# Optimization experiments

Measured on AMD Instinct MI355X. Metric: run time of the kernel, lower is better.

## Reference

```python
import jax, jax.numpy as jnp
import numpy as np

A = 4096      # alleles
RPA = 20      # mean reads per allele
R = A * RPA   # total reads per data source
C = 12        # input channels (pileup features)
L = 32        # read window length
D = 32        # hidden feature dim
NOUT = 2


def setup_inputs() -> dict:
    key = jax.random.key(0)
    k = jax.random.split(key, 8)
    # ragged read counts per allele (alternating 16/24, mean 20, sums to R)
    counts0 = np.tile(np.array([16, 24], dtype=np.int64), A // 2)
    counts1 = np.tile(np.array([24, 16], dtype=np.int64), A // 2)
    return {
        "tensors0": jax.random.normal(k[0], (R, C, L), dtype=jnp.float32),
        "tensors1": jax.random.normal(k[1], (R, C, L), dtype=jnp.float32),
        "W0": jax.random.normal(k[2], (D, C), dtype=jnp.float32) * 0.1,
        "b0": jnp.zeros((D,), dtype=jnp.float32),
        "W1": jax.random.normal(k[3], (D, C), dtype=jnp.float32) * 0.1,
        "b1": jnp.zeros((D,), dtype=jnp.float32),
        "W2": jax.random.normal(k[4], (NOUT, 2 * D), dtype=jnp.float32) * 0.1,
        "b2": jnp.zeros((NOUT,), dtype=jnp.float32),
        "numReadsPerAllele0": jnp.asarray(counts0),
        "numReadsPerAllele1": jnp.asarray(counts1),
        "numAllelesPerSite": jnp.full((A // 2,), 2, dtype=jnp.int64),
        "depthMultiplier0": jnp.asarray(counts0, dtype=jnp.float32),
        "depthMultiplier1": jnp.asarray(counts1, dtype=jnp.float32),
    }


def _frames(t, W, b):
    # pointwise read-feature extractor: [R,C,L] -> [R,D,L]
    return jax.nn.relu(jnp.einsum('rcl,dc->rdl', t, W) + b[None, :, None])


def reference(tensors0, tensors1, W0, b0, W1, b1, W2, b2,
              numReadsPerAllele0, numReadsPerAllele1,
              numAllelesPerSite, depthMultiplier0, depthMultiplier1):
    nA = numReadsPerAllele0.shape[0]
    nR = tensors0.shape[0]
    # segment ids replace torch.split + per-segment torch.sum (ragged segment-sum)
    seg0 = jnp.repeat(jnp.arange(nA), numReadsPerAllele0, total_repeat_length=nR)
    seg1 = jnp.repeat(jnp.arange(nA), numReadsPerAllele1, total_repeat_length=nR)

    frames0 = _frames(tensors0, W0, b0)  # [R,D,L]
    frames1 = _frames(tensors1, W1, b1)

    red0 = jax.ops.segment_sum(frames0, seg0, num_segments=nA)  # [A,D,L]
    red1 = jax.ops.segment_sum(frames1, seg1, num_segments=nA)

    # depth normalization (normalize() in the original)
    red0 = red0 / depthMultiplier0[:, None, None]
    red1 = red1 / depthMultiplier1[:, None, None]

    reduced = jnp.concatenate((red0, red1), axis=1)  # [A, 2D, L]

    # network2 (GraphSearcher): site-specific head modeled as pool + linear
    pooled = jnp.mean(reduced, axis=2)               # [A, 2D]
    return pooled @ W2.T + b2                        # [A, NOUT]
```

## Files before the change

### kernel.cpp

```cpp
#include <hip/hip_runtime.h>

#define A_ALLELES 4096
#define CCH 12
#define LW 32
#define DH 32

__global__ __launch_bounds__(256) void scan_kernel(
    const int* __restrict__ c0, const int* __restrict__ c1,
    int* __restrict__ o0, int* __restrict__ o1)
{
    const int* c = (blockIdx.x == 0) ? c0 : c1;
    int*       o = (blockIdx.x == 0) ? o0 : o1;

    __shared__ int part[256];
    const int tid  = threadIdx.x;
    const int base = tid * 16;

    int loc[16];
    int s = 0;
#pragma unroll
    for (int i = 0; i < 16; ++i) { loc[i] = c[base + i]; s += loc[i]; }
    part[tid] = s;
    __syncthreads();

    for (int st = 1; st < 256; st <<= 1) {
        int v = (tid >= st) ? part[tid - st] : 0;
        __syncthreads();
        part[tid] += v;
        __syncthreads();
    }

    int excl = (tid == 0) ? 0 : part[tid - 1];
#pragma unroll
    for (int i = 0; i < 16; ++i) { o[base + i] = excl; excl += loc[i]; }
}

__global__ __launch_bounds__(256, 4) void main_kernel(
    const float* __restrict__ t0, const float* __restrict__ t1,
    const float* __restrict__ W0, const float* __restrict__ b0,
    const float* __restrict__ W1, const float* __restrict__ b1,
    const float* __restrict__ W2, const float* __restrict__ b2,
    const int*  __restrict__ cnt0, const int* __restrict__ cnt1,
    const float* __restrict__ dm0, const float* __restrict__ dm1,
    const int*  __restrict__ offs0, const int* __restrict__ offs1,
    float* __restrict__ out)
{
    __shared__ float sW2[2 * 2 * DH];
    __shared__ float sB2[2];

    const int tid = threadIdx.x;
    if (tid < 2 * 2 * DH) sW2[tid] = W2[tid];
    if (tid < 2) sB2[tid] = b2[tid];
    __syncthreads();

    const int wave = tid >> 6;
    const int lane = tid & 63;
    const int src  = blockIdx.x >> 10;
    const int a    = ((blockIdx.x & 1023) << 2) | wave;

    const float* __restrict__ tens = src ? t1 : t0;
    const int*   __restrict__ cnt  = src ? cnt1 : cnt0;
    const int*   __restrict__ offs = src ? offs1 : offs0;
    const float* __restrict__ dm   = src ? dm1 : dm0;
    const float* __restrict__ gW   = src ? W1 : W0;
    const float* __restrict__ gB   = src ? b1 : b0;

    const int n     = cnt[a];
    const int start = offs[a];
    const float* base = tens + (size_t)start * (CCH * LW);

    float acc[DH];
#pragma unroll
    for (int d = 0; d < DH; ++d) acc[d] = 0.f;

    const int tasks = n * (LW / 4);
    for (int tsk = lane; tsk < tasks; tsk += 64) {
        const float* rp = base + (size_t)(tsk >> 3) * (CCH * LW) + (tsk & 7) * 4;
        float4 v[CCH];
#pragma unroll
        for (int c = 0; c < CCH; ++c)
            v[c] = *(const float4*)(rp + c * LW);

#pragma unroll
        for (int d = 0; d < DH; ++d) {
            const float bb = gB[d];
            float x0 = bb, x1 = bb, x2 = bb, x3 = bb;
#pragma unroll
            for (int c = 0; c < CCH; ++c) {
                const float wv = gW[d * CCH + c];
                x0 = fmaf(v[c].x, wv, x0);
                x1 = fmaf(v[c].y, wv, x1);
                x2 = fmaf(v[c].z, wv, x2);
                x3 = fmaf(v[c].w, wv, x3);
            }
            acc[d] += (fmaxf(x0, 0.f) + fmaxf(x1, 0.f)) +
                      (fmaxf(x2, 0.f) + fmaxf(x3, 0.f));
        }
    }

#pragma unroll
    for (int d = 0; d < DH; ++d) {
#pragma unroll
        for (int m = 32; m >= 1; m >>= 1)
            acc[d] += __shfl_xor(acc[d], m, 64);
    }

    const float scale = 1.f / (32.f * dm[a]);
    if (lane == 0) {
        float p0 = 0.f, p1 = 0.f;
#pragma unroll
        for (int d = 0; d < DH; ++d) {
            const float pv = acc[d] * scale;
            p0 = fmaf(pv, sW2[0 * 2 * DH + src * DH + d], p0);
            p1 = fmaf(pv, sW2[1 * 2 * DH + src * DH + d], p1);
        }
        if (src == 0) { p0 += sB2[0]; p1 += sB2[1]; }
        atomicAdd(&out[a * 2 + 0], p0);
        atomicAdd(&out[a * 2 + 1], p1);
    }
}

extern "C" void kernel_launch(void* const* d_in, const int* in_sizes, int n_in,
                              void* d_out, int out_size, void* d_ws, size_t ws_size,
                              hipStream_t stream) {
    const float* t0  = (const float*)d_in[0];
    const float* t1  = (const float*)d_in[1];
    const float* W0  = (const float*)d_in[2];
    const float* b0  = (const float*)d_in[3];
    const float* W1  = (const float*)d_in[4];
    const float* b1  = (const float*)d_in[5];
    const float* W2  = (const float*)d_in[6];
    const float* b2  = (const float*)d_in[7];
    const int*  cnt0 = (const int*)d_in[8];
    const int*  cnt1 = (const int*)d_in[9];
    const float* dm0 = (const float*)d_in[11];
    const float* dm1 = (const float*)d_in[12];

    int* offs0 = (int*)d_ws;
    int* offs1 = offs0 + A_ALLELES;

    hipMemsetAsync(d_out, 0, (size_t)out_size * sizeof(float), stream);
    scan_kernel<<<2, 256, 0, stream>>>(cnt0, cnt1, offs0, offs1);

    main_kernel<<<2048, 256, 0, stream>>>(
        t0, t1, W0, b0, W1, b1, W2, b2,
        cnt0, cnt1, dm0, dm1, offs0, offs1, (float*)d_out);
}
```

Before: 324.0 us.

## Compute per-read feature projection with bf16 MFMA instead of scalar FMAs

```diff
diff --git a/kernel.cpp b/kernel.cpp
--- a/kernel.cpp
+++ b/kernel.cpp
@@ -4,6 +4,17 @@
 #define CCH 12
 #define LW 32
 #define DH 32
+#define RDF (CCH * LW)
+#define LANES 64
+
+typedef __attribute__((ext_vector_type(8))) short bf16x8;
+typedef __attribute__((ext_vector_type(4))) float f32x4;
+
+__device__ inline short f2bf(float f) {
+    union { float f; unsigned u; } x; x.f = f;
+    unsigned r = (x.u + 0x7fffu + ((x.u >> 16) & 1u)) >> 16;
+    return (short)r;
+}
 
 __global__ __launch_bounds__(256) void scan_kernel(
     const int* __restrict__ c0, const int* __restrict__ c1,
@@ -45,6 +56,7 @@
     const int*  __restrict__ offs0, const int* __restrict__ offs1,
     float* __restrict__ out)
 {
+    __shared__ float stage[4][RDF];
     __shared__ float sW2[2 * 2 * DH];
     __shared__ float sB2[2];
 
@@ -53,10 +65,10 @@
     if (tid < 2) sB2[tid] = b2[tid];
     __syncthreads();
 
-    const int wave = tid >> 6;
+    const int w    = tid >> 6;
     const int lane = tid & 63;
     const int src  = blockIdx.x >> 10;
-    const int a    = ((blockIdx.x & 1023) << 2) | wave;
+    const int a    = ((blockIdx.x & 1023) << 2) | w;
 
     const float* __restrict__ tens = src ? t1 : t0;
     const int*   __restrict__ cnt  = src ? cnt1 : cnt0;
@@ -65,58 +77,91 @@
     const float* __restrict__ gW   = src ? W1 : W0;
     const float* __restrict__ gB   = src ? b1 : b0;
 
+    const int q  = lane >> 4;
+    const int m  = lane & 15;
+
+    bf16x8 bf0, bf1;
+#pragma unroll
+    for (int j = 0; j < 8; ++j) {
+        const int c  = q * 8 + j;
+        const int cs = (c < CCH) ? c : 0;
+        const float w0v = gW[m * CCH + cs];
+        const float w1v = gW[(16 + m) * CCH + cs];
+        bf0[j] = (c < CCH) ? f2bf(w0v) : (short)0;
+        bf1[j] = (c < CCH) ? f2bf(w1v) : (short)0;
+    }
+    const float bv0 = gB[m], bv1 = gB[16 + m];
+    const f32x4 cb0 = { bv0, bv0, bv0, bv0 };
+    const f32x4 cb1 = { bv1, bv1, bv1, bv1 };
+
     const int n     = cnt[a];
     const int start = offs[a];
-    const float* base = tens + (size_t)start * (CCH * LW);
+    const float* base = tens + (size_t)start * RDF;
 
-    float acc[DH];
+    float acc0 = 0.f, acc1 = 0.f;
+
+    float4 pfA = *(const float4*)(base + lane * 4);
+    float2 pfB = *(const float2*)(base + 256 + lane * 2);
+
+    for (int r = 0; r < n; ++r) {
+        const float4 cA = pfA;
+        const float2 cB = pfB;
+        if (r + 1 < n) {
+            const float* np = base + (size_t)(r + 1) * RDF;
+            pfA = *(const float4*)(np + lane * 4);
+            pfB = *(const float2*)(np + 256 + lane * 2);
+        }
+        *(float4*)&stage[w][lane * 4]       = cA;
+        *(float2*)&stage[w][256 + lane * 2] = cB;
+
+        bf16x8 a0, a1;
 #pragma unroll
-    for (int d = 0; d < DH; ++d) acc[d] = 0.f;
+        for (int j = 0; j < 8; ++j) {
+            const int c  = q * 8 + j;
+            int cc = (q & 1) * 8 + j;
+            if (cc > CCH - 1) cc = CCH - 1;
+            const float v0 = stage[w][cc * LW + m];
+            const float v1 = stage[w][cc * LW + 16 + m];
+            a0[j] = (c < CCH) ? f2bf(v0) : (short)0;
+            a1[j] = (c < CCH) ? f2bf(v1) : (short)0;
+        }
 
-    const int tasks = n * (LW / 4);
-    for (int tsk = lane; tsk < tasks; tsk += 64) {
-        const float* rp = base + (size_t)(tsk >> 3) * (CCH * LW) + (tsk & 7) * 4;
-        float4 v[CCH];
-#pragma unroll
-        for (int c = 0; c < CCH; ++c)
-            v[c] = *(const float4*)(rp + c * LW);
+        const f32x4 d00 = __builtin_amdgcn_mfma_f32_16x16x32_bf16(a0, bf0, cb0, 0, 0, 0);
+        const f32x4 d01 = __builtin_amdgcn_mfma_f32_16x16x32_bf16(a0, bf1, cb1, 0, 0, 0);
+        const f32x4 d10 = __builtin_amdgcn_mfma_f32_16x16x32_bf16(a1, bf0, cb0, 0, 0, 0);
+        const f32x4 d11 = __builtin_amdgcn_mfma_f32_16x16x32_bf16(a1, bf1, cb1, 0, 0, 0);
 
 #pragma unroll
-        for (int d = 0; d < DH; ++d) {
-            const float bb = gB[d];
-            float x0 = bb, x1 = bb, x2 = bb, x3 = bb;
-#pragma unroll
-            for (int c = 0; c < CCH; ++c) {
-                const float wv = gW[d * CCH + c];
-                x0 = fmaf(v[c].x, wv, x0);
-                x1 = fmaf(v[c].y, wv, x1);
-                x2 = fmaf(v[c].z, wv, x2);
-                x3 = fmaf(v[c].w, wv, x3);
-            }
-            acc[d] += (fmaxf(x0, 0.f) + fmaxf(x1, 0.f)) +
-                      (fmaxf(x2, 0.f) + fmaxf(x3, 0.f));
+        for (int k = 0; k < 4; ++k) {
+            acc0 += fmaxf(d00[k], 0.f) + fmaxf(d10[k], 0.f);
+            acc1 += fmaxf(d01[k], 0.f) + fmaxf(d11[k], 0.f);
         }
     }
 
-#pragma unroll
-    for (int d = 0; d < DH; ++d) {
-#pragma unroll
-        for (int m = 32; m >= 1; m >>= 1)
-            acc[d] += __shfl_xor(acc[d], m, 64);
-    }
+    acc0 += __shfl_xor(acc0, 16, 64);
+    acc0 += __shfl_xor(acc0, 32, 64);
+    acc1 += __shfl_xor(acc1, 16, 64);
+    acc1 += __shfl_xor(acc1, 32, 64);
 
     const float scale = 1.f / (32.f * dm[a]);
-    if (lane == 0) {
-        float p0 = 0.f, p1 = 0.f;
+    const float p0 = acc0 * scale;
+    const float p1 = acc1 * scale;
+
+    if (lane < 16) {
+        float c0 = p0 * sW2[0 * 2 * DH + src * DH + m]
+                 + p1 * sW2[0 * 2 * DH + src * DH + 16 + m];
+        float c1 = p0 * sW2[1 * 2 * DH + src * DH + m]
+                 + p1 * sW2[1 * 2 * DH + src * DH + 16 + m];
 #pragma unroll
-        for (int d = 0; d < DH; ++d) {
-            const float pv = acc[d] * scale;
-            p0 = fmaf(pv, sW2[0 * 2 * DH + src * DH + d], p0);
-            p1 = fmaf(pv, sW2[1 * 2 * DH + src * DH + d], p1);
+        for (int mm = 1; mm < 16; mm <<= 1) {
+            c0 += __shfl_xor(c0, mm, 64);
+            c1 += __shfl_xor(c1, mm, 64);
         }
-        if (src == 0) { p0 += sB2[0]; p1 += sB2[1]; }
-        atomicAdd(&out[a * 2 + 0], p0);
-        atomicAdd(&out[a * 2 + 1], p1);
+        if (lane == 0) {
+            if (src == 0) { c0 += sB2[0]; c1 += sB2[1]; }
+            atomicAdd(&out[a * 2 + 0], c0);
+            atomicAdd(&out[a * 2 + 1], c1);
+        }
     }
 }
 
```

Result: faster. 301.8 us (-6.8%).

## Compute per-read feature projection with bf16 MFMA instead of scalar FMAs

Applied to the files above, without the earlier changes.

```diff
diff --git a/kernel.cpp b/kernel.cpp
--- a/kernel.cpp
+++ b/kernel.cpp
@@ -4,6 +4,15 @@
 #define CCH 12
 #define LW 32
 #define DH 32
+#define RDF (CCH * LW)
+
+typedef __attribute__((ext_vector_type(8))) short bf16x8;
+typedef __attribute__((ext_vector_type(4))) float f32x4;
+
+__device__ inline unsigned pk2(float fa, float fb) {
+    const unsigned a = __float_as_uint(fa), b = __float_as_uint(fb);
+    return ((a + 0x8000u) >> 16) | ((b + 0x8000u) & 0xffff0000u);
+}
 
 __global__ __launch_bounds__(256) void scan_kernel(
     const int* __restrict__ c0, const int* __restrict__ c1,
@@ -53,10 +62,10 @@
     if (tid < 2) sB2[tid] = b2[tid];
     __syncthreads();
 
-    const int wave = tid >> 6;
+    const int w    = tid >> 6;
     const int lane = tid & 63;
     const int src  = blockIdx.x >> 10;
-    const int a    = ((blockIdx.x & 1023) << 2) | wave;
+    const int a    = ((blockIdx.x & 1023) << 2) | w;
 
     const float* __restrict__ tens = src ? t1 : t0;
     const int*   __restrict__ cnt  = src ? cnt1 : cnt0;
@@ -65,58 +74,95 @@
     const float* __restrict__ gW   = src ? W1 : W0;
     const float* __restrict__ gB   = src ? b1 : b0;
 
+    const int q = lane >> 4;
+    const int m = lane & 15;
+
+    union { bf16x8 h; unsigned u[4]; } A0, A1;
+    unsigned msk[4];
+#pragma unroll
+    for (int p = 0; p < 4; ++p) {
+        const int c0 = q * 8 + 2 * p, c1 = c0 + 1;
+        msk[p] = (c0 < CCH ? 0x0000ffffu : 0u) | (c1 < CCH ? 0xffff0000u : 0u);
+        const int s0 = (c0 < CCH) ? c0 : 0, s1 = (c1 < CCH) ? c1 : 0;
+        A0.u[p] = pk2(gW[m * CCH + s0],        gW[m * CCH + s1])        & msk[p];
+        A1.u[p] = pk2(gW[(16 + m) * CCH + s0], gW[(16 + m) * CCH + s1]) & msk[p];
+    }
+    f32x4 cb0, cb1;
+#pragma unroll
+    for (int k = 0; k < 4; ++k) {
+        cb0[k] = gB[q * 4 + k];
+        cb1[k] = gB[16 + q * 4 + k];
+    }
+    int off[8];
+#pragma unroll
+    for (int j = 0; j < 8; ++j) {
+        int c = q * 8 + j;
+        if (c > CCH - 1) c = CCH - 1;
+        off[j] = c * LW + m;
+    }
+
     const int n     = cnt[a];
     const int start = offs[a];
-    const float* base = tens + (size_t)start * (CCH * LW);
+    const float* rbase = tens + (size_t)start * RDF;
 
-    float acc[DH];
+    float acc0[4] = {0.f, 0.f, 0.f, 0.f};
+    float acc1[4] = {0.f, 0.f, 0.f, 0.f};
+
+#pragma unroll 2
+    for (int r = 0; r < n; ++r) {
+        float v0[8], v1[8];
 #pragma unroll
-    for (int d = 0; d < DH; ++d) acc[d] = 0.f;
+        for (int j = 0; j < 8; ++j) {
+            v0[j] = rbase[off[j]];
+            v1[j] = rbase[off[j] + 16];
+        }
+        union { bf16x8 h; unsigned u[4]; } B0, B1;
+#pragma unroll
+        for (int p = 0; p < 4; ++p) {
+            B0.u[p] = pk2(v0[2 * p], v0[2 * p + 1]) & msk[p];
+            B1.u[p] = pk2(v1[2 * p], v1[2 * p + 1]) & msk[p];
+        }
 
-    const int tasks = n * (LW / 4);
-    for (int tsk = lane; tsk < tasks; tsk += 64) {
-        const float* rp = base + (size_t)(tsk >> 3) * (CCH * LW) + (tsk & 7) * 4;
-        float4 v[CCH];
-#pragma unroll
-        for (int c = 0; c < CCH; ++c)
-            v[c] = *(const float4*)(rp + c * LW);
+        const f32x4 d00 = __builtin_amdgcn_mfma_f32_16x16x32_bf16(A0.h, B0.h, cb0, 0, 0, 0);
+        const f32x4 d01 = __builtin_amdgcn_mfma_f32_16x16x32_bf16(A0.h, B1.h, cb0, 0, 0, 0);
+        const f32x4 d10 = __builtin_amdgcn_mfma_f32_16x16x32_bf16(A1.h, B0.h, cb1, 0, 0, 0);
+        const f32x4 d11 = __builtin_amdgcn_mfma_f32_16x16x32_bf16(A1.h, B1.h, cb1, 0, 0, 0);
 
 #pragma unroll
-        for (int d = 0; d < DH; ++d) {
-            const float bb = gB[d];
-            float x0 = bb, x1 = bb, x2 = bb, x3 = bb;
+        for (int k = 0; k < 4; ++k) {
+            acc0[k] += fmaxf(d00[k], 0.f) + fmaxf(d01[k], 0.f);
+            acc1[k] += fmaxf(d10[k], 0.f) + fmaxf(d11[k], 0.f);
+        }
+        rbase += RDF;
+    }
+
 #pragma unroll
-            for (int c = 0; c < CCH; ++c) {
-                const float wv = gW[d * CCH + c];
-                x0 = fmaf(v[c].x, wv, x0);
-                x1 = fmaf(v[c].y, wv, x1);
-                x2 = fmaf(v[c].z, wv, x2);
-                x3 = fmaf(v[c].w, wv, x3);
-            }
-            acc[d] += (fmaxf(x0, 0.f) + fmaxf(x1, 0.f)) +
-                      (fmaxf(x2, 0.f) + fmaxf(x3, 0.f));
+    for (int k = 0; k < 4; ++k) {
+#pragma unroll
+        for (int mm = 1; mm < 16; mm <<= 1) {
+            acc0[k] += __shfl_xor(acc0[k], mm, 64);
+            acc1[k] += __shfl_xor(acc1[k], mm, 64);
         }
     }
 
+    const float scale = 1.f / (32.f * dm[a]);
+    float c0 = 0.f, c1 = 0.f;
 #pragma unroll
-    for (int d = 0; d < DH; ++d) {
-#pragma unroll
-        for (int m = 32; m >= 1; m >>= 1)
-            acc[d] += __shfl_xor(acc[d], m, 64);
+    for (int k = 0; k < 4; ++k) {
+        const float p0 = acc0[k] * scale;
+        const float p1 = acc1[k] * scale;
+        c0 += p0 * sW2[0 * 2 * DH + src * DH + q * 4 + k]
+            + p1 * sW2[0 * 2 * DH + src * DH + 16 + q * 4 + k];
+        c1 += p0 * sW2[1 * 2 * DH + src * DH + q * 4 + k]
+            + p1 * sW2[1 * 2 * DH + src * DH + 16 + q * 4 + k];
     }
+    c0 += __shfl_xor(c0, 16, 64); c0 += __shfl_xor(c0, 32, 64);
+    c1 += __shfl_xor(c1, 16, 64); c1 += __shfl_xor(c1, 32, 64);
 
-    const float scale = 1.f / (32.f * dm[a]);
     if (lane == 0) {
-        float p0 = 0.f, p1 = 0.f;
-#pragma unroll
-        for (int d = 0; d < DH; ++d) {
-            const float pv = acc[d] * scale;
-            p0 = fmaf(pv, sW2[0 * 2 * DH + src * DH + d], p0);
-            p1 = fmaf(pv, sW2[1 * 2 * DH + src * DH + d], p1);
-        }
-        if (src == 0) { p0 += sB2[0]; p1 += sB2[1]; }
-        atomicAdd(&out[a * 2 + 0], p0);
-        atomicAdd(&out[a * 2 + 1], p1);
+        if (src == 0) { c0 += sB2[0]; c1 += sB2[1]; }
+        atomicAdd(&out[a * 2 + 0], c0);
+        atomicAdd(&out[a * 2 + 1], c1);
     }
 }
 
```

Result: faster. 301.8 us (-6.8%).

## Compute per-read channel projection with bf16 MFMA and double-buffered loads

Applied to the files above, without the earlier changes.

```diff
diff --git a/kernel.cpp b/kernel.cpp
--- a/kernel.cpp
+++ b/kernel.cpp
@@ -4,6 +4,15 @@
 #define CCH 12
 #define LW 32
 #define DH 32
+#define RDF (CCH * LW)
+
+typedef __attribute__((ext_vector_type(8)))  short bf16x8;
+typedef __attribute__((ext_vector_type(16))) float f32x16;
+
+__device__ inline unsigned pk2(float fa, float fb) {
+    const unsigned a = __float_as_uint(fa), b = __float_as_uint(fb);
+    return ((a + 0x8000u) >> 16) | ((b + 0x8000u) & 0xffff0000u);
+}
 
 __global__ __launch_bounds__(256) void scan_kernel(
     const int* __restrict__ c0, const int* __restrict__ c1,
@@ -53,10 +62,10 @@
     if (tid < 2) sB2[tid] = b2[tid];
     __syncthreads();
 
-    const int wave = tid >> 6;
+    const int w    = tid >> 6;
     const int lane = tid & 63;
     const int src  = blockIdx.x >> 10;
-    const int a    = ((blockIdx.x & 1023) << 2) | wave;
+    const int a    = ((blockIdx.x & 1023) << 2) | w;
 
     const float* __restrict__ tens = src ? t1 : t0;
     const int*   __restrict__ cnt  = src ? cnt1 : cnt0;
@@ -65,59 +74,117 @@
     const float* __restrict__ gW   = src ? W1 : W0;
     const float* __restrict__ gB   = src ? b1 : b0;
 
+    const int l = lane & 31;
+    const int h = lane >> 5;
+
+    union { bf16x8 v; unsigned u[4]; } Af;
+#pragma unroll
+    for (int p = 0; p < 4; ++p) {
+        const int c0 = h * 8 + 2 * p, c1 = c0 + 1;
+        const float f0 = (c0 < CCH) ? gW[l * CCH + c0] : 0.f;
+        const float f1 = (c1 < CCH) ? gW[l * CCH + c1] : 0.f;
+        Af.u[p] = pk2(f0, f1);
+    }
+    f32x16 cb;
+#pragma unroll
+    for (int reg = 0; reg < 16; ++reg)
+        cb[reg] = gB[(reg & 3) + 8 * (reg >> 2) + 4 * h];
+
     const int n     = cnt[a];
     const int start = offs[a];
-    const float* base = tens + (size_t)start * (CCH * LW);
-
-    float acc[DH];
-#pragma unroll
-    for (int d = 0; d < DH; ++d) acc[d] = 0.f;
-
-    const int tasks = n * (LW / 4);
-    for (int tsk = lane; tsk < tasks; tsk += 64) {
-        const float* rp = base + (size_t)(tsk >> 3) * (CCH * LW) + (tsk & 7) * 4;
-        float4 v[CCH];
-#pragma unroll
-        for (int c = 0; c < CCH; ++c)
-            v[c] = *(const float4*)(rp + c * LW);
-
-#pragma unroll
-        for (int d = 0; d < DH; ++d) {
-            const float bb = gB[d];
-            float x0 = bb, x1 = bb, x2 = bb, x3 = bb;
-#pragma unroll
-            for (int c = 0; c < CCH; ++c) {
-                const float wv = gW[d * CCH + c];
-                x0 = fmaf(v[c].x, wv, x0);
-                x1 = fmaf(v[c].y, wv, x1);
-                x2 = fmaf(v[c].z, wv, x2);
-                x3 = fmaf(v[c].w, wv, x3);
+    const float* rb = tens + (size_t)start * RDF;
+
+    const float* pLo = rb + l + h * 256;
+    const float* pHi = rb + l + (h ? 256 : 128);
+
+    float acc[16];
+#pragma unroll
+    for (int reg = 0; reg < 16; ++reg) acc[reg] = 0.f;
+
+#define LOAD8(buf, P, W_)  do {                                     \
+        buf[0] = pLo[(P) + 0];  buf[1] = pLo[(P) + 32];             \
+        buf[2] = pLo[(P) + 64]; buf[3] = pLo[(P) + 96];             \
+        buf[4] = pHi[(P) + 0];  buf[5] = pHi[(P) + 32];             \
+        buf[6] = pHi[(P) + 64]; buf[7] = pHi[(P) + 96]; } while (0)
+
+#define PACK_MFMA_ACC(buf) do {                                     \
+        union { bf16x8 v; unsigned u[4]; } Bf;                      \
+        Bf.u[0] = pk2(buf[0], buf[1]); Bf.u[1] = pk2(buf[2], buf[3]); \
+        Bf.u[2] = pk2(buf[4], buf[5]); Bf.u[3] = pk2(buf[6], buf[7]); \
+        const f32x16 D = __builtin_amdgcn_mfma_f32_32x32x16_bf16(   \
+            Af.v, Bf.v, cb, 0, 0, 0);                               \
+        _Pragma("unroll")                                           \
+        for (int reg = 0; reg < 16; ++reg)                          \
+            acc[reg] += fmaxf(D[reg], 0.f); } while (0)
+
+    const int n2 = n & ~1;
+    if (n2 >= 2) {
+        float bA[8], bB[8];
+        LOAD8(bA, 0, 0);
+        LOAD8(bB, 384, 0);
+        const int iters = (n2 - 2) >> 1;
+        for (int it = 0; it < iters; ++it) {
+            {
+                union { bf16x8 v; unsigned u[4]; } Bf;
+                Bf.u[0] = pk2(bA[0], bA[1]); Bf.u[1] = pk2(bA[2], bA[3]);
+                Bf.u[2] = pk2(bA[4], bA[5]); Bf.u[3] = pk2(bA[6], bA[7]);
+                LOAD8(bA, 768, 0);
+                const f32x16 D = __builtin_amdgcn_mfma_f32_32x32x16_bf16(
+                    Af.v, Bf.v, cb, 0, 0, 0);
+#pragma unroll
+                for (int reg = 0; reg < 16; ++reg) acc[reg] += fmaxf(D[reg], 0.f);
+                pLo += 384; pHi += 384;
             }
-            acc[d] += (fmaxf(x0, 0.f) + fmaxf(x1, 0.f)) +
-                      (fmaxf(x2, 0.f) + fmaxf(x3, 0.f));
+            {
+                union { bf16x8 v; unsigned u[4]; } Bf;
+                Bf.u[0] = pk2(bB[0], bB[1]); Bf.u[1] = pk2(bB[2], bB[3]);
+                Bf.u[2] = pk2(bB[4], bB[5]); Bf.u[3] = pk2(bB[6], bB[7]);
+                LOAD8(bB, 768, 0);
+                const f32x16 D = __builtin_amdgcn_mfma_f32_32x32x16_bf16(
+                    Af.v, Bf.v, cb, 0, 0, 0);
+#pragma unroll
+                for (int reg = 0; reg < 16; ++reg) acc[reg] += fmaxf(D[reg], 0.f);
+                pLo += 384; pHi += 384;
+            }
         }
-    }
-
-#pragma unroll
-    for (int d = 0; d < DH; ++d) {
-#pragma unroll
-        for (int m = 32; m >= 1; m >>= 1)
-            acc[d] += __shfl_xor(acc[d], m, 64);
+        PACK_MFMA_ACC(bA);
+        PACK_MFMA_ACC(bB);
+    }
+    if (n & 1) {
+        const float* qLo = rb + (size_t)(n - 1) * RDF + l + h * 256;
+        const float* qHi = rb + (size_t)(n - 1) * RDF + l + (h ? 256 : 128);
+        float bT[8];
+        bT[0] = qLo[0];  bT[1] = qLo[32]; bT[2] = qLo[64]; bT[3] = qLo[96];
+        bT[4] = qHi[0];  bT[5] = qHi[32]; bT[6] = qHi[64]; bT[7] = qHi[96];
+        PACK_MFMA_ACC(bT);
+    }
+
+#pragma unroll
+    for (int reg = 0; reg < 16; ++reg) {
+#pragma unroll
+        for (int mm = 1; mm < 32; mm <<= 1)
+            acc[reg] += __shfl_xor(acc[reg], mm, 64);
     }
 
     const float scale = 1.f / (32.f * dm[a]);
+    float c0s = 0.f, c1s = 0.f;
+#pragma unroll
+    for (int reg = 0; reg < 16; ++reg) {
+        const int d = (reg & 3) + 8 * (reg >> 2) + 4 * h;
+        const float pv = acc[reg] * scale;
+        c0s = fmaf(pv, sW2[0 * 2 * DH + src * DH + d], c0s);
+        c1s = fmaf(pv, sW2[1 * 2 * DH + src * DH + d], c1s);
+    }
+    c0s += __shfl_xor(c0s, 32, 64);
+    c1s += __shfl_xor(c1s, 32, 64);
+
     if (lane == 0) {
-        float p0 = 0.f, p1 = 0.f;
-#pragma unroll
-        for (int d = 0; d < DH; ++d) {
-            const float pv = acc[d] * scale;
-            p0 = fmaf(pv, sW2[0 * 2 * DH + src * DH + d], p0);
-            p1 = fmaf(pv, sW2[1 * 2 * DH + src * DH + d], p1);
-        }
-        if (src == 0) { p0 += sB2[0]; p1 += sB2[1]; }
-        atomicAdd(&out[a * 2 + 0], p0);
-        atomicAdd(&out[a * 2 + 1], p1);
-    }
+        if (src == 0) { c0s += sB2[0]; c1s += sB2[1]; }
+        atomicAdd(&out[a * 2 + 0], c0s);
+        atomicAdd(&out[a * 2 + 1], c1s);
+    }
+#undef LOAD8
+#undef PACK_MFMA_ACC
 }
 
 extern "C" void kernel_launch(void* const* d_in, const int* in_sizes, int n_in,
```

New measurement: 295.2 us. 1.1x faster.
